# Optimization experiments

Hardware: AMD Instinct MI355X
Metric: run time of the kernel (lower is better)

Reference implementation:

```python
import jax, jax.numpy as jnp
import numpy as np

N_NODES = 50000
N_EDGES = 800000
N_GRAPHS = 128
IN_CH, HIDDEN, OUT_CH = 16, 64, 2


def gcn_conv(x, src, dst, W, b, n_nodes):
    """GCNConv: add self-loops, sym-normalized adjacency scatter-add, linear."""
    h = x @ W  # [N, H]
    loop = jnp.arange(n_nodes, dtype=src.dtype)
    s = jnp.concatenate([src, loop])  # [E+N]
    d = jnp.concatenate([dst, loop])
    deg = jax.ops.segment_sum(jnp.ones_like(d, dtype=h.dtype), d, num_segments=n_nodes)
    dinv = jnp.where(deg > 0, jax.lax.rsqrt(deg), 0.0)  # deg^{-1/2}
    norm = dinv[s] * dinv[d]  # [E+N]
    msg = h[s] * norm[:, None]  # gather + scale, [E+N, H]
    out = jax.ops.segment_sum(msg, d, num_segments=n_nodes)  # scatter-add
    return out + b


def global_mean_pool(x, batch, n_graphs):
    sums = jax.ops.segment_sum(x, batch, num_segments=n_graphs)
    cnts = jax.ops.segment_sum(jnp.ones((x.shape[0],), x.dtype), batch, num_segments=n_graphs)
    return sums / jnp.maximum(cnts, 1.0)[:, None]


def setup_inputs() -> dict:
    key = jax.random.key(0)
    ks = jax.random.split(key, 10)
    x = jax.random.normal(ks[0], (N_NODES, IN_CH), dtype=jnp.float32)
    edge_index = jax.random.randint(ks[1], (2, N_EDGES), 0, N_NODES, dtype=jnp.int64)
    batch = jnp.sort(jax.random.randint(ks[2], (N_NODES,), 0, N_GRAPHS, dtype=jnp.int64))
    def glorot(k, shp):
        lim = float(np.sqrt(6.0 / (shp[0] + shp[1])))
        return jax.random.uniform(k, shp, jnp.float32, -lim, lim)
    W1 = glorot(ks[3], (IN_CH, HIDDEN))
    b1 = jnp.zeros((HIDDEN,), jnp.float32)
    W2 = glorot(ks[4], (HIDDEN, HIDDEN))
    b2 = jnp.zeros((HIDDEN,), jnp.float32)
    Wc = glorot(ks[5], (HIDDEN, OUT_CH))
    bc = jnp.zeros((OUT_CH,), jnp.float32)
    return {"x": x, "edge_index": edge_index, "batch": batch,
            "W1": W1, "b1": b1, "W2": W2, "b2": b2, "Wc": Wc, "bc": bc}


def reference(x, edge_index, batch, W1, b1, W2, b2, Wc, bc):
    src, dst = edge_index[0], edge_index[1]
    n = x.shape[0]
    h = jax.nn.relu(gcn_conv(x, src, dst, W1, b1, n))
    # dropout p=0.3 is identity in eval mode
    h = jax.nn.relu(gcn_conv(h, src, dst, W2, b2, n))
    g = global_mean_pool(h, batch, N_GRAPHS)  # [G, H]
    return g @ Wc + bc  # [G, out_channels]
```

## Files before the change

### kernel.cpp

```cpp
#include <hip/hip_runtime.h>
#include <hip/hip_bf16.h>

#define N_NODES 50000
#define N_EDGES 800000
#define N_GRAPHS 128
#define IN_CH 16
#define HIDDEN 64
#define OUT_CH 2

#define BSHIFT 7
#define BNODES 128
#define NB ((N_NODES + BNODES - 1) / BNODES)
#define BCAP 3072
#define ECHUNK 4096
#define EB ((N_EDGES + ECHUNK - 1) / ECHUNK)
#define MAXK 12
#define EPT 16
#define WT1_LD 18
#define AGG_LD 72
#define W2T_ENT (HIDDEN * AGG_LD)

typedef __attribute__((ext_vector_type(8))) short bf16x8;
typedef __attribute__((ext_vector_type(4))) float f32x4;

__device__ __forceinline__ float bf2f(unsigned short u) {
    return __uint_as_float(((unsigned)u) << 16);
}
__device__ __forceinline__ unsigned short f2bf(float f) {
    __hip_bfloat16 h = __float2bfloat16(f);
    return *reinterpret_cast<unsigned short*>(&h);
}


__global__ void bucket_scatter_kernel(const int* __restrict__ src, const int* __restrict__ dst,
                                      int* __restrict__ bh, int* __restrict__ bh2,
                                      int* __restrict__ pairs,
                                      const float* __restrict__ W2, unsigned short* __restrict__ w2t) {
    __shared__ int lh[NB];
    __shared__ int lstart[NB];
    __shared__ int spair[256];
    int t = threadIdx.x;
    if (blockIdx.x == 0) {
        for (int i = t; i < HIDDEN * HIDDEN; i += 256) {
            int k = i >> 6, c = i & 63;
            w2t[c * AGG_LD + k] = f2bf(W2[i]);
        }
    }
    for (int i = t; i < NB; i += 256) lh[i] = 0;
    __syncthreads();

    int base = blockIdx.x * ECHUNK;
    int nE = N_EDGES - base;
    if (nE > ECHUNK) nE = ECHUNK;

    int ed[EPT], es[EPT];
#pragma unroll
    for (int k = 0; k < EPT; k++) {
        int i = k * 256 + t;
        if (i < nE) {
            ed[k] = dst[base + i];
            es[k] = src[base + i];
        } else {
            ed[k] = -1;
            es[k] = 0;
        }
    }
#pragma unroll
    for (int k = 0; k < EPT; k++)
        if ((unsigned)ed[k] < N_NODES) atomicAdd(&lh[ed[k] >> BSHIFT], 1);
    __syncthreads();

    int a0 = (2 * t < NB) ? lh[2 * t] : 0;
    int a1 = (2 * t + 1 < NB) ? lh[2 * t + 1] : 0;
    spair[t] = a0 + a1;
    __syncthreads();
    for (int off = 1; off < 256; off <<= 1) {
        int u = (t >= off) ? spair[t - off] : 0;
        __syncthreads();
        spair[t] += u;
        __syncthreads();
    }
    int ex = spair[t] - (a0 + a1);
    if (2 * t < NB) lstart[2 * t] = ex;
    if (2 * t + 1 < NB) lstart[2 * t + 1] = ex + a0;
    __syncthreads();

    for (int i = t; i < NB; i += 256) {
        bh[i * EB + blockIdx.x] = lh[i];
        bh2[i * EB + blockIdx.x] = base + lstart[i];
        lh[i] = 0;
    }
    __syncthreads();

#pragma unroll
    for (int k = 0; k < EPT; k++) {
        if ((unsigned)ed[k] < N_NODES) {
            int b = ed[k] >> BSHIFT;
            int r = atomicAdd(&lh[b], 1);
            pairs[base + lstart[b] + r] = (es[k] << BSHIFT) | (ed[k] & (BNODES - 1));
        }
    }
}


__global__ void bucket_csr_kernel(const int* __restrict__ pairs, const int* __restrict__ bh,
                                  const int* __restrict__ bh2,
                                  int* __restrict__ csr, int* __restrict__ rowptr,
                                  int* __restrict__ cnt_node, float* __restrict__ dinv,
                                  const float* __restrict__ x, unsigned short* __restrict__ xs,
                                  float* __restrict__ sums, float* __restrict__ cntg) {
    __shared__ int segaddr[EB];
    __shared__ int pref[EB];
    __shared__ int ptmp[256];
    __shared__ int lcnt[BNODES];
    __shared__ int lsc[BNODES];
    __shared__ int lrow[BNODES];
    __shared__ float sdv[BNODES];
    int b = blockIdx.x;
    int t = threadIdx.x;

    if (b == 0) {
        for (int i = t; i < N_GRAPHS * HIDDEN; i += 256) sums[i] = 0.0f;
        if (t < N_GRAPHS) cntg[t] = 0.0f;
    }

    int cntv = (t < EB) ? bh[b * EB + t] : 0;
    if (t < EB) segaddr[t] = bh2[b * EB + t];
    if (t < BNODES) lcnt[t] = 0;
    ptmp[t] = cntv;
    __syncthreads();
    for (int off = 1; off < 256; off <<= 1) {
        int u = (t >= off) ? ptmp[t - off] : 0;
        __syncthreads();
        ptmp[t] += u;
        __syncthreads();
    }
    if (t < EB) pref[t] = ptmp[t];
    __syncthreads();
    int K = pref[EB - 1];
    if (K > BCAP) K = BCAP;

    int myp[MAXK], myr[MAXK];
#pragma unroll
    for (int k = 0; k < MAXK; k++) {
        int i = k * 256 + t;
        myp[k] = -1;
        if (i < K) {
            int lo = 0, hi = EB - 1;
            while (lo < hi) {
                int mid = (lo + hi) >> 1;
                if (pref[mid] > i) hi = mid; else lo = mid + 1;
            }
            int excl = (lo > 0) ? pref[lo - 1] : 0;
            int p = pairs[segaddr[lo] + (i - excl)];
            myp[k] = p;
            myr[k] = atomicAdd(&lcnt[p & (BNODES - 1)], 1);
        }
    }
    __syncthreads();
    if (t < BNODES) lsc[t] = lcnt[t];
    __syncthreads();
    for (int off = 1; off < BNODES; off <<= 1) {
        int u = (t >= off && t < BNODES) ? lsc[t - off] : 0;
        __syncthreads();
        if (t < BNODES) lsc[t] += u;
        __syncthreads();
    }
    int bstart = b * BCAP;
    if (t < BNODES) {
        int ex = lsc[t] - lcnt[t];
        lrow[t] = ex;
        float dv = rsqrtf((float)(lcnt[t] + 1));
        sdv[t] = dv;
        int n = b * BNODES + t;
        if (n < N_NODES) {
            rowptr[n] = bstart + ex;
            cnt_node[n] = lcnt[t];
            dinv[n] = dv;
        }
    }
    __syncthreads();
#pragma unroll
    for (int k = 0; k < MAXK; k++) {
        if (myp[k] >= 0)
            csr[bstart + lrow[myp[k] & (BNODES - 1)] + myr[k]] = myp[k] >> BSHIFT;
    }
    for (int i = t; i < BNODES * IN_CH; i += 256) {
        int nl = i >> 4;
        int n = b * BNODES + nl;
        if (n < N_NODES) xs[n * IN_CH + (i & 15)] = f2bf(sdv[nl] * x[n * IN_CH + (i & 15)]);
    }
}


__global__ void fused_l1_kernel(const unsigned short* __restrict__ xs, const int* __restrict__ csr_src,
                                const int* __restrict__ rowptr, const int* __restrict__ cnt,
                                const float* __restrict__ dinv, const float* __restrict__ W,
                                const float* __restrict__ b, __hip_bfloat16* __restrict__ h) {
    __shared__ float sWT[HIDDEN * WT1_LD];
    __shared__ float sx[16 * IN_CH];
    int t = threadIdx.x;
    for (int i = t; i < IN_CH * HIDDEN; i += 256) {
        int k = i >> 6, c = i & 63;
        sWT[c * WT1_LD + k] = W[i];
    }

    int n0 = blockIdx.x * 16;
    int w = t >> 6;
    int lane = t & 63;
    int e16 = lane >> 2;
    int cc = (lane & 3) * 4;

    int lens[4], starts[4];
#pragma unroll
    for (int q = 0; q < 4; q++) {
        int n = n0 + w * 4 + q;
        lens[q] = cnt[n];
        starts[q] = rowptr[n];
    }

    for (int q = 0; q < 4; q++) {
        int row = w * 4 + q;
        int n = n0 + row;
        int len = lens[q];
        int start = starts[q];
        int last = len - 1;
        int iters = (len + 31) >> 5;
        float4 acc = make_float4(0.f, 0.f, 0.f, 0.f);
        for (int m = 0; m < iters; m++) {
            int base = m * 32 + e16;
#pragma unroll
            for (int k = 0; k < 2; k++) {
                int j = base + 16 * k;
                int jj = j <= last ? j : last;
                float msk = j <= last ? 1.0f : 0.0f;
                int s = csr_src[start + jj];
                ushort4 xv = *(const ushort4*)&xs[s * IN_CH + cc];
                acc.x += msk * bf2f(xv.x);
                acc.y += msk * bf2f(xv.y);
                acc.z += msk * bf2f(xv.z);
                acc.w += msk * bf2f(xv.w);
            }
        }
#pragma unroll
        for (int m = 4; m <= 32; m <<= 1) {
            acc.x += __shfl_xor(acc.x, m, 64);
            acc.y += __shfl_xor(acc.y, m, 64);
            acc.z += __shfl_xor(acc.z, m, 64);
            acc.w += __shfl_xor(acc.w, m, 64);
        }
        if (lane < 4) {
            float dn = dinv[n];
            ushort4 xsv = *(const ushort4*)&xs[n * IN_CH + cc];
            float4 v;
            v.x = dn * (acc.x + bf2f(xsv.x));
            v.y = dn * (acc.y + bf2f(xsv.y));
            v.z = dn * (acc.z + bf2f(xsv.z));
            v.w = dn * (acc.w + bf2f(xsv.w));
            *(float4*)&sx[row * IN_CH + cc] = v;
        }
    }
    __syncthreads();

    int r = w;
    int c = t & 63;
    float bias = b[c];
#pragma unroll
    for (int nb = 0; nb < 4; nb++) {
        int row = nb * 4 + r;
        int n = n0 + row;
        if (n >= N_NODES) continue;
        float acch = bias;
#pragma unroll
        for (int k4 = 0; k4 < IN_CH; k4 += 4) {
            float4 a = *(const float4*)&sx[row * IN_CH + k4];
            float2 w0 = *(const float2*)&sWT[c * WT1_LD + k4];
            float2 w1 = *(const float2*)&sWT[c * WT1_LD + k4 + 2];
            acch += a.x * w0.x + a.y * w0.y + a.z * w1.x + a.w * w1.y;
        }
        float v = acch > 0.0f ? acch : 0.0f;
        h[n * HIDDEN + c] = __float2bfloat16(dinv[n] * v);
    }
}


__global__ void fused_l2_kernel(const __hip_bfloat16* __restrict__ h, const int* __restrict__ csr_src,
                                const int* __restrict__ rowptr, const int* __restrict__ cnt,
                                const float* __restrict__ dinv, const unsigned short* __restrict__ w2t,
                                const float* __restrict__ b, const int* __restrict__ batch,
                                float* __restrict__ sums, float* __restrict__ cntg) {
    __shared__ unsigned short sW[W2T_ENT];
    __shared__ unsigned short sagg[16 * AGG_LD];
    int t = threadIdx.x;
    {
        const uint4* wp = (const uint4*)w2t;
        uint4* sWv = (uint4*)sW;
#pragma unroll
        for (int i = 0; i < 3; i++) {
            int idx = i * 256 + t;
            if (idx < W2T_ENT / 8) sWv[idx] = wp[idx];
        }
    }

    int n0 = blockIdx.x * 16;
    int w = t >> 6;
    int lane = t & 63;
    int e8 = lane >> 3;
    int cc8 = (lane & 7) * 8;
    const unsigned short* hu = (const unsigned short*)h;

    int lens[4], starts[4];
#pragma unroll
    for (int q = 0; q < 4; q++) {
        int n = n0 + w * 4 + q;
        lens[q] = cnt[n];
        starts[q] = rowptr[n];
    }

    for (int q = 0; q < 4; q++) {
        int row = w * 4 + q;
        int n = n0 + row;
        int len = lens[q];
        int start = starts[q];
        int last = len - 1;
        int iters = (len + 31) >> 5;
        float4 alo = make_float4(0.f, 0.f, 0.f, 0.f);
        float4 ahi = make_float4(0.f, 0.f, 0.f, 0.f);
        for (int m = 0; m < iters; m++) {
            int base = m * 32 + e8;
#pragma unroll
            for (int k = 0; k < 4; k++) {
                int j = base + 8 * k;
                int jj = j <= last ? j : last;
                float msk = j <= last ? 1.0f : 0.0f;
                int s = csr_src[start + jj];
                uint4 raw = *(const uint4*)&hu[s * HIDDEN + cc8];
                alo.x += msk * __uint_as_float(raw.x << 16);
                alo.y += msk * __uint_as_float(raw.x & 0xffff0000u);
                alo.z += msk * __uint_as_float(raw.y << 16);
                alo.w += msk * __uint_as_float(raw.y & 0xffff0000u);
                ahi.x += msk * __uint_as_float(raw.z << 16);
                ahi.y += msk * __uint_as_float(raw.z & 0xffff0000u);
                ahi.z += msk * __uint_as_float(raw.w << 16);
                ahi.w += msk * __uint_as_float(raw.w & 0xffff0000u);
            }
        }
#pragma unroll
        for (int m = 8; m <= 32; m <<= 1) {
            alo.x += __shfl_xor(alo.x, m, 64);
            alo.y += __shfl_xor(alo.y, m, 64);
            alo.z += __shfl_xor(alo.z, m, 64);
            alo.w += __shfl_xor(alo.w, m, 64);
            ahi.x += __shfl_xor(ahi.x, m, 64);
            ahi.y += __shfl_xor(ahi.y, m, 64);
            ahi.z += __shfl_xor(ahi.z, m, 64);
            ahi.w += __shfl_xor(ahi.w, m, 64);
        }
        if (lane < 8) {
            uint4 sv = *(const uint4*)&hu[n * HIDDEN + cc8];
            float dn = dinv[n];
            ushort4 o0, o1;
            o0.x = f2bf(dn * (alo.x + __uint_as_float(sv.x << 16)));
            o0.y = f2bf(dn * (alo.y + __uint_as_float(sv.x & 0xffff0000u)));
            o0.z = f2bf(dn * (alo.z + __uint_as_float(sv.y << 16)));
            o0.w = f2bf(dn * (alo.w + __uint_as_float(sv.y & 0xffff0000u)));
            o1.x = f2bf(dn * (ahi.x + __uint_as_float(sv.z << 16)));
            o1.y = f2bf(dn * (ahi.y + __uint_as_float(sv.z & 0xffff0000u)));
            o1.z = f2bf(dn * (ahi.z + __uint_as_float(sv.w << 16)));
            o1.w = f2bf(dn * (ahi.w + __uint_as_float(sv.w & 0xffff0000u)));
            *(ushort4*)&sagg[row * AGG_LD + cc8] = o0;
            *(ushort4*)&sagg[row * AGG_LD + cc8 + 4] = o1;
        }
    }
    __syncthreads();

    int quad = lane >> 4;
    int col = lane & 15;
    int cch = w * 16 + col;
    bf16x8 a0 = *(const bf16x8*)&sagg[col * AGG_LD + quad * 8];
    bf16x8 a1 = *(const bf16x8*)&sagg[col * AGG_LD + 32 + quad * 8];
    bf16x8 b0 = *(const bf16x8*)&sW[cch * AGG_LD + quad * 8];
    bf16x8 b1 = *(const bf16x8*)&sW[cch * AGG_LD + 32 + quad * 8];
    f32x4 d = {0.f, 0.f, 0.f, 0.f};
    d = __builtin_amdgcn_mfma_f32_16x16x32_bf16(a0, b0, d, 0, 0, 0);
    d = __builtin_amdgcn_mfma_f32_16x16x32_bf16(a1, b1, d, 0, 0, 0);
    float bias = b[cch];
    float v[4];
#pragma unroll
    for (int r = 0; r < 4; r++) {
        float z = d[r] + bias;
        v[r] = z > 0.0f ? z : 0.0f;
    }

    int glo = batch[n0];
    int ghi = batch[n0 + 15];
    if (glo == ghi) {
        float s4 = (v[0] + v[1]) + (v[2] + v[3]);
        s4 += __shfl_xor(s4, 16, 64);
        s4 += __shfl_xor(s4, 32, 64);
        if (quad == 0) atomicAdd(&sums[glo * HIDDEN + cch], s4);
        if (t == 0) atomicAdd(&cntg[glo], 16.0f);
    } else {
#pragma unroll
        for (int r = 0; r < 4; r++) {
            int g = batch[n0 + quad * 4 + r];
            if ((unsigned)g < N_GRAPHS) atomicAdd(&sums[g * HIDDEN + cch], v[r]);
        }
        if (w == 0 && col == 0) {
#pragma unroll
            for (int r = 0; r < 4; r++) {
                int g = batch[n0 + quad * 4 + r];
                if ((unsigned)g < N_GRAPHS) atomicAdd(&cntg[g], 1.0f);
            }
        }
    }
}


__global__ void head_kernel(const float* __restrict__ sums, const float* __restrict__ cntg,
                            const float* __restrict__ Wc, const float* __restrict__ bc,
                            float* __restrict__ out) {
    int t = blockIdx.x * blockDim.x + threadIdx.x;
    if (t >= N_GRAPHS * OUT_CH) return;
    int g = t >> 1;
    int o = t & 1;
    float inv = 1.0f / fmaxf(cntg[g], 1.0f);
    float acc = bc[o];
#pragma unroll
    for (int k = 0; k < HIDDEN; k++) acc += sums[g * HIDDEN + k] * inv * Wc[k * OUT_CH + o];
    out[t] = acc;
}


extern "C" void kernel_launch(void* const* d_in, const int* in_sizes, int n_in,
                              void* d_out, int out_size, void* d_ws, size_t ws_size,
                              hipStream_t stream) {
    const float* x  = (const float*)d_in[0];
    const int* ei   = (const int*)d_in[1];
    const int* bat  = (const int*)d_in[2];
    const float* W1 = (const float*)d_in[3];
    const float* b1 = (const float*)d_in[4];
    const float* W2 = (const float*)d_in[5];
    const float* b2 = (const float*)d_in[6];
    const float* Wc = (const float*)d_in[7];
    const float* bc = (const float*)d_in[8];
    float* out = (float*)d_out;

    const int* src = ei;
    const int* dst = ei + N_EDGES;

    char* ws = (char*)d_ws;
    size_t off = 0;
    auto carve = [&](size_t nbytes) {
        char* p = ws + off;
        off += (nbytes + 255) & ~(size_t)255;
        return p;
    };
    float* sums     = (float*)carve(N_GRAPHS * HIDDEN * sizeof(float));
    float* cntg     = (float*)carve(N_GRAPHS * sizeof(float));
    unsigned short* w2t = (unsigned short*)carve(W2T_ENT * sizeof(unsigned short));
    int*   bh       = (int*)carve((size_t)NB * EB * sizeof(int));
    int*   bh2      = (int*)carve((size_t)NB * EB * sizeof(int));
    int*   pairs    = (int*)carve((size_t)EB * ECHUNK * sizeof(int));
    int*   csr      = (int*)carve((size_t)NB * BCAP * sizeof(int));
    int*   rowptr   = (int*)carve(N_NODES * sizeof(int));
    int*   cnt_node = (int*)carve(N_NODES * sizeof(int));
    float* dinv     = (float*)carve(N_NODES * sizeof(float));
    unsigned short* xs = (unsigned short*)carve((size_t)N_NODES * IN_CH * sizeof(unsigned short));
    __hip_bfloat16* bufA = (__hip_bfloat16*)carve((size_t)N_NODES * HIDDEN * sizeof(__hip_bfloat16));
    (void)ws_size;

    const int node16Blk = (N_NODES + 15) / 16;

    bucket_scatter_kernel<<<EB, 256, 0, stream>>>(src, dst, bh, bh2, pairs, W2, w2t);
    bucket_csr_kernel<<<NB, 256, 0, stream>>>(pairs, bh, bh2, csr, rowptr, cnt_node, dinv,
                                              x, xs, sums, cntg);
    fused_l1_kernel<<<node16Blk, 256, 0, stream>>>(xs, csr, rowptr, cnt_node, dinv, W1, b1, bufA);
    fused_l2_kernel<<<node16Blk, 256, 0, stream>>>(bufA, csr, rowptr, cnt_node, dinv, w2t, b2,
                                                   bat, sums, cntg);
    head_kernel<<<1, 256, 0, stream>>>(sums, cntg, Wc, bc, out);
}
```

Measured before the change: 164.7 us.

## Fuse pooling and classifier head into layer-2 kernel, precompute graph counts

Graph node counts are now computed in the CSR-build kernel, using per-block shared histograms flushed with global atomics. The linear head is folded into the layer-2 epilogue: each wave projects its pooled features onto the two output channels, scales by the inverse count, and atomically adds into the output, which is pre-initialised with the bias. This drops the separate head kernel and the 128x64 sums buffer and cuts atomic traffic from 64 to 2 values per graph update. The cost is extra shuffles per wave and nondeterministic float summation order in the output.

```diff
diff --git a/kernel.cpp b/kernel.cpp
--- a/kernel.cpp
+++ b/kernel.cpp
@@ -35,7 +35,9 @@
 __global__ void bucket_scatter_kernel(const int* __restrict__ src, const int* __restrict__ dst,
                                       int* __restrict__ bh, int* __restrict__ bh2,
                                       int* __restrict__ pairs,
-                                      const float* __restrict__ W2, unsigned short* __restrict__ w2t) {
+                                      const float* __restrict__ W2, unsigned short* __restrict__ w2t,
+                                      float* __restrict__ cntg, const float* __restrict__ bc,
+                                      float* __restrict__ out) {
     __shared__ int lh[NB];
     __shared__ int lstart[NB];
     __shared__ int spair[256];
@@ -45,6 +47,8 @@
             int k = i >> 6, c = i & 63;
             w2t[c * AGG_LD + k] = f2bf(W2[i]);
         }
+        if (t < N_GRAPHS) cntg[t] = 0.0f;
+        if (t < N_GRAPHS * OUT_CH) out[t] = bc[t & 1];
     }
     for (int i = t; i < NB; i += 256) lh[i] = 0;
     __syncthreads();
@@ -108,7 +112,7 @@
                                   int* __restrict__ csr, int* __restrict__ rowptr,
                                   int* __restrict__ cnt_node, float* __restrict__ dinv,
                                   const float* __restrict__ x, unsigned short* __restrict__ xs,
-                                  float* __restrict__ sums, float* __restrict__ cntg) {
+                                  const int* __restrict__ batch, float* __restrict__ cntg) {
     __shared__ int segaddr[EB];
     __shared__ int pref[EB];
     __shared__ int ptmp[256];
@@ -116,17 +120,14 @@
     __shared__ int lsc[BNODES];
     __shared__ int lrow[BNODES];
     __shared__ float sdv[BNODES];
+    __shared__ int lgc[N_GRAPHS];
     int b = blockIdx.x;
     int t = threadIdx.x;
-
-    if (b == 0) {
-        for (int i = t; i < N_GRAPHS * HIDDEN; i += 256) sums[i] = 0.0f;
-        if (t < N_GRAPHS) cntg[t] = 0.0f;
-    }
 
     int cntv = (t < EB) ? bh[b * EB + t] : 0;
     if (t < EB) segaddr[t] = bh2[b * EB + t];
     if (t < BNODES) lcnt[t] = 0;
+    if (t < N_GRAPHS) lgc[t] = 0;
     ptmp[t] = cntv;
     __syncthreads();
     for (int off = 1; off < 256; off <<= 1) {
@@ -177,6 +178,7 @@
             rowptr[n] = bstart + ex;
             cnt_node[n] = lcnt[t];
             dinv[n] = dv;
+            atomicAdd(&lgc[batch[n]], 1);
         }
     }
     __syncthreads();
@@ -190,6 +192,8 @@
         int n = b * BNODES + nl;
         if (n < N_NODES) xs[n * IN_CH + (i & 15)] = f2bf(sdv[nl] * x[n * IN_CH + (i & 15)]);
     }
+    for (int i = t; i < N_GRAPHS; i += 256)
+        if (lgc[i] > 0) atomicAdd(&cntg[i], (float)lgc[i]);
 }
 
 
@@ -288,7 +292,8 @@
                                 const int* __restrict__ rowptr, const int* __restrict__ cnt,
                                 const float* __restrict__ dinv, const unsigned short* __restrict__ w2t,
                                 const float* __restrict__ b, const int* __restrict__ batch,
-                                float* __restrict__ sums, float* __restrict__ cntg) {
+                                const float* __restrict__ cntg, const float* __restrict__ Wc,
+                                float* __restrict__ out) {
     __shared__ unsigned short sW[W2T_ENT];
     __shared__ unsigned short sagg[16 * AGG_LD];
     int t = threadIdx.x;
@@ -392,43 +397,44 @@
         v[r] = z > 0.0f ? z : 0.0f;
     }
 
+    float wc0 = Wc[cch * OUT_CH + 0];
+    float wc1 = Wc[cch * OUT_CH + 1];
     int glo = batch[n0];
     int ghi = batch[n0 + 15];
     if (glo == ghi) {
         float s4 = (v[0] + v[1]) + (v[2] + v[3]);
         s4 += __shfl_xor(s4, 16, 64);
         s4 += __shfl_xor(s4, 32, 64);
-        if (quad == 0) atomicAdd(&sums[glo * HIDDEN + cch], s4);
-        if (t == 0) atomicAdd(&cntg[glo], 16.0f);
+        float inv = 1.0f / fmaxf(cntg[glo], 1.0f);
+        float p0 = s4 * wc0;
+        float p1 = s4 * wc1;
+#pragma unroll
+        for (int m = 1; m <= 8; m <<= 1) {
+            p0 += __shfl_xor(p0, m, 64);
+            p1 += __shfl_xor(p1, m, 64);
+        }
+        if (lane == 0) {
+            atomicAdd(&out[glo * OUT_CH + 0], p0 * inv);
+            atomicAdd(&out[glo * OUT_CH + 1], p1 * inv);
+        }
     } else {
 #pragma unroll
         for (int r = 0; r < 4; r++) {
             int g = batch[n0 + quad * 4 + r];
-            if ((unsigned)g < N_GRAPHS) atomicAdd(&sums[g * HIDDEN + cch], v[r]);
-        }
-        if (w == 0 && col == 0) {
-#pragma unroll
-            for (int r = 0; r < 4; r++) {
-                int g = batch[n0 + quad * 4 + r];
-                if ((unsigned)g < N_GRAPHS) atomicAdd(&cntg[g], 1.0f);
+            float inv = 1.0f / fmaxf(cntg[g], 1.0f);
+            float p0 = v[r] * wc0;
+            float p1 = v[r] * wc1;
+#pragma unroll
+            for (int m = 1; m <= 8; m <<= 1) {
+                p0 += __shfl_xor(p0, m, 64);
+                p1 += __shfl_xor(p1, m, 64);
             }
-        }
-    }
-}
-
-
-__global__ void head_kernel(const float* __restrict__ sums, const float* __restrict__ cntg,
-                            const float* __restrict__ Wc, const float* __restrict__ bc,
-                            float* __restrict__ out) {
-    int t = blockIdx.x * blockDim.x + threadIdx.x;
-    if (t >= N_GRAPHS * OUT_CH) return;
-    int g = t >> 1;
-    int o = t & 1;
-    float inv = 1.0f / fmaxf(cntg[g], 1.0f);
-    float acc = bc[o];
-#pragma unroll
-    for (int k = 0; k < HIDDEN; k++) acc += sums[g * HIDDEN + k] * inv * Wc[k * OUT_CH + o];
-    out[t] = acc;
+            if (col == 0) {
+                atomicAdd(&out[g * OUT_CH + 0], p0 * inv);
+                atomicAdd(&out[g * OUT_CH + 1], p1 * inv);
+            }
+        }
+    }
 }
 
 
@@ -456,7 +462,6 @@
         off += (nbytes + 255) & ~(size_t)255;
         return p;
     };
-    float* sums     = (float*)carve(N_GRAPHS * HIDDEN * sizeof(float));
     float* cntg     = (float*)carve(N_GRAPHS * sizeof(float));
     unsigned short* w2t = (unsigned short*)carve(W2T_ENT * sizeof(unsigned short));
     int*   bh       = (int*)carve((size_t)NB * EB * sizeof(int));
@@ -472,11 +477,11 @@
 
     const int node16Blk = (N_NODES + 15) / 16;
 
-    bucket_scatter_kernel<<<EB, 256, 0, stream>>>(src, dst, bh, bh2, pairs, W2, w2t);
+    bucket_scatter_kernel<<<EB, 256, 0, stream>>>(src, dst, bh, bh2, pairs, W2, w2t,
+                                                  cntg, bc, out);
     bucket_csr_kernel<<<NB, 256, 0, stream>>>(pairs, bh, bh2, csr, rowptr, cnt_node, dinv,
-                                              x, xs, sums, cntg);
+                                              x, xs, bat, cntg);
     fused_l1_kernel<<<node16Blk, 256, 0, stream>>>(xs, csr, rowptr, cnt_node, dinv, W1, b1, bufA);
     fused_l2_kernel<<<node16Blk, 256, 0, stream>>>(bufA, csr, rowptr, cnt_node, dinv, w2t, b2,
-                                                   bat, sums, cntg);
-    head_kernel<<<1, 256, 0, stream>>>(sums, cntg, Wc, bc, out);
-}
+                                                   bat, cntg, Wc, out);
+}
```

New measurement: 257.4 us. 56.3% more time.
